# Kernel optimization log

Measured on AMD Instinct MI355X. Metric: run time of the kernel, lower is better.

The kernel has to match this reference:

```python
import jax, jax.numpy as jnp
import numpy as np

N0, N1 = 25000, 25000
N = N0 + N1
E = 600000
D = 128          # in = lattern = hidden = out channels
R = 4            # relations per conv (num_relations // 2)
NB = 4           # num_bases per conv
EPS = 1e-5


def setup_inputs() -> dict:
    key = jax.random.key(0)
    ks = jax.random.split(key, 24)
    inp = {}
    inp['x0'] = jax.random.normal(ks[0], (N0, 128), dtype=jnp.float32)
    inp['x1'] = jax.random.normal(ks[1], (N1, 256), dtype=jnp.float32)
    inp['edge_index'] = jax.random.randint(ks[2], (2, E), 0, N, dtype=jnp.int64)
    inp['edge_type'] = jax.random.randint(ks[3], (E,), 0, 2 * R, dtype=jnp.int64)
    # per-type input projections (torch Linear: y = x @ W.T + b)
    inp['lin0_w'] = jax.random.normal(ks[4], (D, 128), dtype=jnp.float32) * (1.0 / np.sqrt(128))
    inp['lin0_b'] = jnp.zeros((D,), dtype=jnp.float32)
    inp['lin1_w'] = jax.random.normal(ks[5], (D, 256), dtype=jnp.float32) * (1.0 / np.sqrt(256))
    inp['lin1_b'] = jnp.zeros((D,), dtype=jnp.float32)
    # 3 RGCN convs with basis decomposition: weight[r] = sum_b comp[r,b] * bases[b]
    for i, k0 in zip((1, 2, 3), (6, 10, 14)):
        inp[f'comp{i}'] = jax.random.normal(ks[k0], (R, NB), dtype=jnp.float32) * (1.0 / np.sqrt(NB))
        inp[f'bases{i}'] = jax.random.normal(ks[k0 + 1], (NB, D, D), dtype=jnp.float32) * (1.0 / np.sqrt(D))
        inp[f'root{i}'] = jax.random.normal(ks[k0 + 2], (D, D), dtype=jnp.float32) * (1.0 / np.sqrt(D))
        inp[f'b{i}'] = jnp.zeros((D,), dtype=jnp.float32)
    inp['gamma'] = jnp.ones((D,), dtype=jnp.float32)
    inp['beta'] = jnp.zeros((D,), dtype=jnp.float32)
    return inp


def _rgcn_conv(x, src, dst, rel, comp, bases, root, bias):
    # weight: [R, D_in, D_out] via basis decomposition
    W = jnp.einsum('rb,bio->rio', comp, bases)
    out = x @ root + bias  # root/self transform
    xs = x[src]            # [E, D_in] gather (shared across relations)
    for r in range(R):     # small fixed relation count
        mask = (rel == r)
        msg = (xs @ W[r]) * mask[:, None].astype(x.dtype)
        s = jax.ops.segment_sum(msg, dst, num_segments=x.shape[0])
        cnt = jax.ops.segment_sum(mask.astype(x.dtype), dst, num_segments=x.shape[0])
        out = out + s / jnp.maximum(cnt, 1.0)[:, None]  # per-relation scatter-mean
    return out


def reference(x0, x1, edge_index, edge_type,
              lin0_w, lin0_b, lin1_w, lin1_b,
              comp1, bases1, root1, b1,
              comp2, bases2, root2, b2,
              comp3, bases3, root3, b3,
              gamma, beta):
    # trans_dimensions: project each node-type feature matrix, concat on node dim
    x = jnp.concatenate([x0 @ lin0_w.T + lin0_b, x1 @ lin1_w.T + lin1_b], axis=0)
    src, dst = edge_index[0], edge_index[1]
    rel = edge_type // 2
    x = jax.nn.relu(_rgcn_conv(x, src, dst, rel, comp1, bases1, root1, b1))
    # dropout p=0.1: identity in eval mode
    x = jax.nn.relu(_rgcn_conv(x, src, dst, rel, comp2, bases2, root2, b2))
    # dropout p=0.2: identity in eval mode
    x = _rgcn_conv(x, src, dst, rel, comp3, bases3, root3, b3)
    mu = jnp.mean(x, axis=-1, keepdims=True)
    var = jnp.mean(jnp.square(x - mu), axis=-1, keepdims=True)
    return (x - mu) * jax.lax.rsqrt(var + EPS) * gamma + beta
```

## Files before the change

kernel.cpp:

```cpp
#include <hip/hip_runtime.h>


constexpr int cN0 = 25000;
constexpr int cN1 = 25000;
constexpr int cN  = 50000;
constexpr int cE  = 600000;
constexpr int cD  = 128;
constexpr int cR  = 4;
constexpr int cNB = 4;
constexpr int cRN = cR * cN;
constexpr int cSCANBLK = (cRN + 255) / 256;
constexpr int cK  = 640;
constexpr int cWT = cD * cK;

typedef __attribute__((ext_vector_type(8))) short short8v;
typedef __attribute__((ext_vector_type(4))) float float4v;

__device__ inline float bf_hi(float f, short& h)
{
    unsigned u = __float_as_uint(f);
    unsigned r = (u + 0x7fff + ((u >> 16) & 1)) >> 16;
    h = (short)r;
    return __uint_as_float(r << 16);
}

__global__ __launch_bounds__(256)
void build_wt_kernel(const float* __restrict__ c1, const float* __restrict__ ba1, const float* __restrict__ r1,
                     const float* __restrict__ c2, const float* __restrict__ ba2, const float* __restrict__ r2,
                     const float* __restrict__ c3, const float* __restrict__ ba3, const float* __restrict__ r3,
                     short* __restrict__ wt_hi, short* __restrict__ wt_lo)
{
    int idx = blockIdx.x * 256 + threadIdx.x;
    if (idx >= 3 * cWT) return;
    int layer = idx / cWT;
    int rem   = idx - layer * cWT;
    int k     = rem >> 7;
    int col   = rem & 127;
    const float* comp = (layer == 0) ? c1 : (layer == 1) ? c2 : c3;
    const float* bas  = (layer == 0) ? ba1 : (layer == 1) ? ba2 : ba3;
    const float* root = (layer == 0) ? r1 : (layer == 1) ? r2 : r3;
    float v;
    if (k < 128) {
        v = root[k * 128 + col];
    } else {
        int r = (k - 128) >> 7, kk = (k - 128) & 127;
        v = 0.f;
#pragma unroll
        for (int b = 0; b < cNB; ++b)
            v += comp[r * cNB + b] * bas[b * 16384 + kk * 128 + col];
    }
    short h, l;
    float hf = bf_hi(v, h);
    bf_hi(v - hf, l);
    size_t o = (size_t)layer * cWT + (size_t)col * cK + k;
    wt_hi[o] = h;
    wt_lo[o] = l;
}

__global__ __launch_bounds__(256)
void count_kernel(const int* __restrict__ ei, const int* __restrict__ et,
                  int* __restrict__ cnt)
{
    int t = blockIdx.x * 256 + threadIdx.x;
    if (t >= cE) return;
    int dst = ei[cE + t];
    int rel = et[t] >> 1;
    atomicAdd(&cnt[rel * cN + dst], 1);
}

__global__ __launch_bounds__(256)
void scan1_kernel(const int* __restrict__ cnt, int* __restrict__ offs,
                  int* __restrict__ bsum)
{
    __shared__ int s[256];
    int t = threadIdx.x;
    int i = blockIdx.x * 256 + t;
    int v = (i < cRN) ? cnt[i] : 0;
    s[t] = v;
    __syncthreads();
#pragma unroll
    for (int off = 1; off < 256; off <<= 1) {
        int u = (t >= off) ? s[t - off] : 0;
        __syncthreads();
        s[t] += u;
        __syncthreads();
    }
    if (i < cRN) offs[i] = s[t] - v;
    if (t == 255) bsum[blockIdx.x] = s[255];
}

__global__ __launch_bounds__(1024)
void scan2_kernel(int* __restrict__ bsum)
{
    __shared__ int s[1024];
    int t = threadIdx.x;
    int v = (t < cSCANBLK) ? bsum[t] : 0;
    s[t] = v;
    __syncthreads();
#pragma unroll
    for (int off = 1; off < 1024; off <<= 1) {
        int u = (t >= off) ? s[t - off] : 0;
        __syncthreads();
        s[t] += u;
        __syncthreads();
    }
    if (t < cSCANBLK) bsum[t] = s[t] - v;
}

__global__ __launch_bounds__(256)
void scan3_kernel(int* __restrict__ offs, const int* __restrict__ bsum)
{
    int i = blockIdx.x * 256 + threadIdx.x;
    if (i < cRN) offs[i] += bsum[blockIdx.x];
    if (i == 0) offs[cRN] = cE;
}

__global__ __launch_bounds__(256)
void fill_kernel(const int* __restrict__ ei, const int* __restrict__ et,
                 const int* __restrict__ offs, int* __restrict__ fillpos,
                 int* __restrict__ esorted)
{
    int t = blockIdx.x * 256 + threadIdx.x;
    if (t >= cE) return;
    int src = ei[t];
    int dst = ei[cE + t];
    int rel = et[t] >> 1;
    int g = rel * cN + dst;
    int p = atomicAdd(&fillpos[g], 1);
    esorted[offs[g] + p] = src;
}

__global__ __launch_bounds__(256)
void seg_scatter_kernel(const float* __restrict__ x, const int* __restrict__ esorted,
                        const int* __restrict__ offs, float* __restrict__ agg)
{
    int g = blockIdx.x * 4 + (threadIdx.x >> 6);
    if (g >= cRN) return;
    int lane = threadIdx.x & 63;
    int beg = offs[g], end = offs[g + 1];
    float2 acc = {0.f, 0.f};
    for (int j = beg; j < end; ++j) {
        int src = esorted[j];
        const float2 v = *(const float2*)(x + (size_t)src * cD + lane * 2);
        acc.x += v.x;
        acc.y += v.y;
    }
    float invk = 1.0f / fmaxf((float)(end - beg), 1.0f);
    acc.x *= invk;
    acc.y *= invk;
    *(float2*)(agg + (size_t)g * cD + lane * 2) = acc;
}

template<int EPI>
__global__ __launch_bounds__(512)
void mfma_conv_kernel(const float* __restrict__ x,
                      const float* __restrict__ agg,
                      const short* __restrict__ wt_hi,
                      const short* __restrict__ wt_lo,
                      const float* __restrict__ bias,
                      float* __restrict__ out)
{
    __shared__ short As_hi[128][32];
    __shared__ short As_lo[128][32];
    __shared__ short Bs_hi[128][32];
    __shared__ short Bs_lo[128][32];

    const int tid  = threadIdx.x;
    const int row0 = blockIdx.x * 128;

    const int srow = tid >> 2;
    const int sk8  = (tid & 3) * 8;
    const int gi   = row0 + srow;

    const int lane = tid & 63;
    const int wid  = tid >> 6;
    const int wm   = wid >> 2;
    const int wn   = wid & 3;
    const int fr   = lane & 15;
    const int fk   = (lane >> 4) * 8;

    float4v acc[4][2];
#pragma unroll
    for (int m = 0; m < 4; ++m)
#pragma unroll
        for (int n = 0; n < 2; ++n)
#pragma unroll
            for (int r = 0; r < 4; ++r) acc[m][n][r] = 0.f;

#pragma unroll 1
    for (int st = 0; st < 20; ++st) {
        const int s  = st >> 2;
        const int k0 = (st & 3) * 32;

        short8v vh, vl;
        if (gi < cN) {
            const float* src = (s == 0)
                ? (x + (size_t)gi * cD + k0 + sk8)
                : (agg + ((size_t)(s - 1) * cN + gi) * cD + k0 + sk8);
            float4 a = *(const float4*)(src);
            float4 b = *(const float4*)(src + 4);
            float vv[8] = {a.x, a.y, a.z, a.w, b.x, b.y, b.z, b.w};
#pragma unroll
            for (int j = 0; j < 8; ++j) {
                short h, l;
                float hf = bf_hi(vv[j], h);
                bf_hi(vv[j] - hf, l);
                vh[j] = h;
                vl[j] = l;
            }
        } else {
#pragma unroll
            for (int j = 0; j < 8; ++j) { vh[j] = 0; vl[j] = 0; }
        }
        *(short8v*)&As_hi[srow][sk8] = vh;
        *(short8v*)&As_lo[srow][sk8] = vl;

        const int kglob = st * 32 + sk8;
        *(short8v*)&Bs_hi[srow][sk8] = *(const short8v*)(wt_hi + (size_t)srow * cK + kglob);
        *(short8v*)&Bs_lo[srow][sk8] = *(const short8v*)(wt_lo + (size_t)srow * cK + kglob);

        __syncthreads();

        short8v ah[4], al[4], bh[2], bl[2];
#pragma unroll
        for (int mf = 0; mf < 4; ++mf) {
            ah[mf] = *(const short8v*)&As_hi[wm * 64 + mf * 16 + fr][fk];
            al[mf] = *(const short8v*)&As_lo[wm * 64 + mf * 16 + fr][fk];
        }
#pragma unroll
        for (int nf = 0; nf < 2; ++nf) {
            bh[nf] = *(const short8v*)&Bs_hi[wn * 32 + nf * 16 + fr][fk];
            bl[nf] = *(const short8v*)&Bs_lo[wn * 32 + nf * 16 + fr][fk];
        }

#pragma unroll
        for (int mf = 0; mf < 4; ++mf)
#pragma unroll
            for (int nf = 0; nf < 2; ++nf) {
                acc[mf][nf] = __builtin_amdgcn_mfma_f32_16x16x32_bf16(al[mf], bh[nf], acc[mf][nf], 0, 0, 0);
                acc[mf][nf] = __builtin_amdgcn_mfma_f32_16x16x32_bf16(ah[mf], bl[nf], acc[mf][nf], 0, 0, 0);
                acc[mf][nf] = __builtin_amdgcn_mfma_f32_16x16x32_bf16(ah[mf], bh[nf], acc[mf][nf], 0, 0, 0);
            }

        __syncthreads();
    }

#pragma unroll
    for (int mf = 0; mf < 4; ++mf)
#pragma unroll
        for (int nf = 0; nf < 2; ++nf) {
            int col = wn * 32 + nf * 16 + fr;
            float bi = bias[col];
#pragma unroll
            for (int r = 0; r < 4; ++r) {
                int gr = row0 + wm * 64 + mf * 16 + (lane >> 4) * 4 + r;
                if (gr < cN) {
                    float v = acc[mf][nf][r] + bi;
                    if (EPI == 1) v = fmaxf(v, 0.f);
                    out[(size_t)gr * cD + col] = v;
                }
            }
        }
}

__global__ __launch_bounds__(256)
void ln_kernel(float* __restrict__ io, const float* __restrict__ gamma,
               const float* __restrict__ beta)
{
    int row = blockIdx.x * 4 + (threadIdx.x >> 6);
    if (row >= cN) return;
    int lane = threadIdx.x & 63;
    float2 v = *(const float2*)(io + (size_t)row * cD + lane * 2);
    float sm = v.x + v.y;
#pragma unroll
    for (int off = 1; off < 64; off <<= 1) sm += __shfl_xor(sm, off, 64);
    float mu = sm * (1.0f / 128.0f);
    float dx = v.x - mu, dy = v.y - mu;
    float sq = dx * dx + dy * dy;
#pragma unroll
    for (int off = 1; off < 64; off <<= 1) sq += __shfl_xor(sq, off, 64);
    float rs = rsqrtf(sq * (1.0f / 128.0f) + 1e-5f);
    float2 g = *(const float2*)(gamma + lane * 2);
    float2 b = *(const float2*)(beta + lane * 2);
    float2 o;
    o.x = dx * rs * g.x + b.x;
    o.y = dy * rs * g.y + b.y;
    *(float2*)(io + (size_t)row * cD + lane * 2) = o;
}

template<int NSEG>
__global__ __launch_bounds__(256)
void proj_gemm_kernel(const float* __restrict__ A0,
                      const float* __restrict__ B0,
                      const float* __restrict__ bias,
                      float* __restrict__ out,
                      int M)
{
    __shared__ float As[32][128];
    __shared__ float Bs[32][128];

    const int tid = threadIdx.x;
    const int tx = tid & 15;
    const int ty = tid >> 4;
    const int row0 = blockIdx.x * 128;

    float acc[8][8];
#pragma unroll
    for (int m = 0; m < 8; ++m)
#pragma unroll
        for (int n = 0; n < 8; ++n) acc[m][n] = 0.f;

    const int iloc = tid & 127;
    const int kh   = tid >> 7;
    const int gi   = row0 + iloc;

#pragma unroll 1
    for (int ch = 0; ch < NSEG * 4; ++ch) {
        const int s  = ch >> 2;
        const int k0 = (ch & 3) * 32;

        if (gi < M) {
            const float* src = A0 + (size_t)gi * (NSEG * 128) + s * 128 + k0 + kh * 16;
#pragma unroll
            for (int j = 0; j < 4; ++j) {
                float4 t4 = *(const float4*)(src + j * 4);
                As[kh * 16 + j * 4 + 0][iloc] = t4.x;
                As[kh * 16 + j * 4 + 1][iloc] = t4.y;
                As[kh * 16 + j * 4 + 2][iloc] = t4.z;
                As[kh * 16 + j * 4 + 3][iloc] = t4.w;
            }
        } else {
#pragma unroll
            for (int j = 0; j < 16; ++j) As[kh * 16 + j][iloc] = 0.f;
        }

        {
            const int o = iloc;
            const float* p = B0 + (size_t)o * (NSEG * 128) + s * 128 + k0 + kh * 16;
#pragma unroll
            for (int j = 0; j < 4; ++j) {
                float4 t4 = *(const float4*)(p + j * 4);
                Bs[kh * 16 + j * 4 + 0][o] = t4.x;
                Bs[kh * 16 + j * 4 + 1][o] = t4.y;
                Bs[kh * 16 + j * 4 + 2][o] = t4.z;
                Bs[kh * 16 + j * 4 + 3][o] = t4.w;
            }
        }
        __syncthreads();

#pragma unroll
        for (int kk = 0; kk < 32; ++kk) {
            float a[8], b[8];
            *(float4*)&a[0] = *(const float4*)&As[kk][ty * 8];
            *(float4*)&a[4] = *(const float4*)&As[kk][ty * 8 + 4];
            *(float4*)&b[0] = *(const float4*)&Bs[kk][tx * 8];
            *(float4*)&b[4] = *(const float4*)&Bs[kk][tx * 8 + 4];
#pragma unroll
            for (int m = 0; m < 8; ++m)
#pragma unroll
                for (int n = 0; n < 8; ++n)
                    acc[m][n] = fmaf(a[m], b[n], acc[m][n]);
        }
        __syncthreads();
    }

    float bi[8];
    *(float4*)&bi[0] = *(const float4*)(bias + tx * 8);
    *(float4*)&bi[4] = *(const float4*)(bias + tx * 8 + 4);

#pragma unroll
    for (int m = 0; m < 8; ++m) {
        int gr = row0 + ty * 8 + m;
        if (gr < M) {
            float v[8];
#pragma unroll
            for (int n = 0; n < 8; ++n) v[n] = acc[m][n] + bi[n];
            float4* o0 = (float4*)(out + (size_t)gr * 128 + tx * 8);
            o0[0] = *(float4*)&v[0];
            o0[1] = *(float4*)&v[4];
        }
    }
}

extern "C" void kernel_launch(void* const* d_in, const int* in_sizes, int n_in,
                              void* d_out, int out_size, void* d_ws, size_t ws_size,
                              hipStream_t stream)
{
    (void)in_sizes; (void)n_in; (void)out_size; (void)ws_size;

    const float* x0     = (const float*)d_in[0];
    const float* x1     = (const float*)d_in[1];
    const int*   ei     = (const int*)d_in[2];
    const int*   et     = (const int*)d_in[3];
    const float* lin0_w = (const float*)d_in[4];
    const float* lin0_b = (const float*)d_in[5];
    const float* lin1_w = (const float*)d_in[6];
    const float* lin1_b = (const float*)d_in[7];
    const float* comp1  = (const float*)d_in[8];
    const float* bases1 = (const float*)d_in[9];
    const float* root1  = (const float*)d_in[10];
    const float* b1     = (const float*)d_in[11];
    const float* comp2  = (const float*)d_in[12];
    const float* bases2 = (const float*)d_in[13];
    const float* root2  = (const float*)d_in[14];
    const float* b2     = (const float*)d_in[15];
    const float* comp3  = (const float*)d_in[16];
    const float* bases3 = (const float*)d_in[17];
    const float* root3  = (const float*)d_in[18];
    const float* b3     = (const float*)d_in[19];
    const float* gamma  = (const float*)d_in[20];
    const float* beta   = (const float*)d_in[21];

    float* out = (float*)d_out;

    char* ws = (char*)d_ws;
    size_t off = 0;
    auto alloc = [&](size_t bytes) {
        void* p = ws + off;
        off = (off + bytes + 255) & ~(size_t)255;
        return p;
    };
    float* xbuf    = (float*)alloc((size_t)cN * cD * 4);
    float* agg     = (float*)alloc((size_t)cR * cN * cD * 4);
    short* wt_hi   = (short*)alloc((size_t)3 * cWT * 2);
    short* wt_lo   = (short*)alloc((size_t)3 * cWT * 2);
    int*   offs    = (int*)alloc((size_t)(cRN + 1) * 4);
    int*   cnt     = (int*)alloc((size_t)cRN * 4);
    int*   bsum    = (int*)alloc((size_t)cSCANBLK * 4);
    int*   esorted = (int*)alloc((size_t)cE * 4);

    build_wt_kernel<<<(3 * cWT + 255) / 256, 256, 0, stream>>>(
        comp1, bases1, root1, comp2, bases2, root2, comp3, bases3, root3,
        wt_hi, wt_lo);
    hipMemsetAsync(cnt, 0, (size_t)cRN * 4, stream);
    count_kernel<<<(cE + 255) / 256, 256, 0, stream>>>(ei, et, cnt);
    scan1_kernel<<<cSCANBLK, 256, 0, stream>>>(cnt, offs, bsum);
    scan2_kernel<<<1, 1024, 0, stream>>>(bsum);
    scan3_kernel<<<cSCANBLK, 256, 0, stream>>>(offs, bsum);
    hipMemsetAsync(cnt, 0, (size_t)cRN * 4, stream);
    fill_kernel<<<(cE + 255) / 256, 256, 0, stream>>>(ei, et, offs, cnt, esorted);

    proj_gemm_kernel<1><<<(cN0 + 127) / 128, 256, 0, stream>>>(
        x0, lin0_w, lin0_b, xbuf, cN0);
    proj_gemm_kernel<2><<<(cN1 + 127) / 128, 256, 0, stream>>>(
        x1, lin1_w, lin1_b, xbuf + (size_t)cN0 * cD, cN1);

    const int convGrid = (cN + 127) / 128;

    seg_scatter_kernel<<<(cRN + 3) / 4, 256, 0, stream>>>(xbuf, esorted, offs, agg);
    mfma_conv_kernel<1><<<convGrid, 512, 0, stream>>>(
        xbuf, agg, wt_hi + (size_t)0 * cWT, wt_lo + (size_t)0 * cWT, b1, out);

    seg_scatter_kernel<<<(cRN + 3) / 4, 256, 0, stream>>>(out, esorted, offs, agg);
    mfma_conv_kernel<1><<<convGrid, 512, 0, stream>>>(
        out, agg, wt_hi + (size_t)1 * cWT, wt_lo + (size_t)1 * cWT, b2, xbuf);

    seg_scatter_kernel<<<(cRN + 3) / 4, 256, 0, stream>>>(xbuf, esorted, offs, agg);
    mfma_conv_kernel<0><<<convGrid, 512, 0, stream>>>(
        xbuf, agg, wt_hi + (size_t)2 * cWT, wt_lo + (size_t)2 * cWT, b3, out);
    ln_kernel<<<(cN + 3) / 4, 256, 0, stream>>>(out, gamma, beta);
}
```

Baseline: 647.2 us.

## Batch edge index loads with shuffles and swizzle LDS tiles in MFMA conv

The segment scatter kernel now loads up to 64 source indices at once with one coalesced wave load, broadcasts them with shuffles, and issues four row gathers per iteration. This raises memory-level parallelism and removes the serial index-load dependency. Separately, the MFMA GEMM kernel XOR-swizzles the LDS column offsets for the A and B tiles to cut bank conflicts on the short8 reads. The added shuffles and predicated adds cost a few instructions per edge.

```diff
diff --git a/kernel.cpp b/kernel.cpp
--- a/kernel.cpp
+++ b/kernel.cpp
@@ -138,14 +138,34 @@
     if (g >= cRN) return;
     int lane = threadIdx.x & 63;
     int beg = offs[g], end = offs[g + 1];
+    int n = end - beg;
     float2 acc = {0.f, 0.f};
-    for (int j = beg; j < end; ++j) {
-        int src = esorted[j];
-        const float2 v = *(const float2*)(x + (size_t)src * cD + lane * 2);
-        acc.x += v.x;
-        acc.y += v.y;
-    }
-    float invk = 1.0f / fmaxf((float)(end - beg), 1.0f);
+    const float* xl = x + lane * 2;
+
+    for (int base = 0; base < n; base += 64) {
+        int m = n - base;
+        if (m > 64) m = 64;
+        int idx = (lane < m) ? esorted[beg + base + lane] : 0;
+        for (int jb = 0; jb < m; jb += 4) {
+            int j1 = (jb + 1 < m) ? jb + 1 : jb;
+            int j2 = (jb + 2 < m) ? jb + 2 : jb;
+            int j3 = (jb + 3 < m) ? jb + 3 : jb;
+            int s0 = __shfl(idx, jb, 64);
+            int s1 = __shfl(idx, j1, 64);
+            int s2 = __shfl(idx, j2, 64);
+            int s3 = __shfl(idx, j3, 64);
+            float2 v0 = *(const float2*)(xl + (size_t)s0 * cD);
+            float2 v1 = *(const float2*)(xl + (size_t)s1 * cD);
+            float2 v2 = *(const float2*)(xl + (size_t)s2 * cD);
+            float2 v3 = *(const float2*)(xl + (size_t)s3 * cD);
+            acc.x += v0.x;
+            acc.y += v0.y;
+            if (jb + 1 < m) { acc.x += v1.x; acc.y += v1.y; }
+            if (jb + 2 < m) { acc.x += v2.x; acc.y += v2.y; }
+            if (jb + 3 < m) { acc.x += v3.x; acc.y += v3.y; }
+        }
+    }
+    float invk = 1.0f / fmaxf((float)n, 1.0f);
     acc.x *= invk;
     acc.y *= invk;
     *(float2*)(agg + (size_t)g * cD + lane * 2) = acc;
@@ -170,6 +190,7 @@
 
     const int srow = tid >> 2;
     const int sk8  = (tid & 3) * 8;
+    const int scol = sk8 ^ (((srow >> 1) & 3) << 3);
     const int gi   = row0 + srow;
 
     const int lane = tid & 63;
@@ -212,25 +233,29 @@
 #pragma unroll
             for (int j = 0; j < 8; ++j) { vh[j] = 0; vl[j] = 0; }
         }
-        *(short8v*)&As_hi[srow][sk8] = vh;
-        *(short8v*)&As_lo[srow][sk8] = vl;
+        *(short8v*)&As_hi[srow][scol] = vh;
+        *(short8v*)&As_lo[srow][scol] = vl;
 
         const int kglob = st * 32 + sk8;
-        *(short8v*)&Bs_hi[srow][sk8] = *(const short8v*)(wt_hi + (size_t)srow * cK + kglob);
-        *(short8v*)&Bs_lo[srow][sk8] = *(const short8v*)(wt_lo + (size_t)srow * cK + kglob);
+        *(short8v*)&Bs_hi[srow][scol] = *(const short8v*)(wt_hi + (size_t)srow * cK + kglob);
+        *(short8v*)&Bs_lo[srow][scol] = *(const short8v*)(wt_lo + (size_t)srow * cK + kglob);
 
         __syncthreads();
 
         short8v ah[4], al[4], bh[2], bl[2];
 #pragma unroll
         for (int mf = 0; mf < 4; ++mf) {
-            ah[mf] = *(const short8v*)&As_hi[wm * 64 + mf * 16 + fr][fk];
-            al[mf] = *(const short8v*)&As_lo[wm * 64 + mf * 16 + fr][fk];
+            int arow = wm * 64 + mf * 16 + fr;
+            int acol = fk ^ (((arow >> 1) & 3) << 3);
+            ah[mf] = *(const short8v*)&As_hi[arow][acol];
+            al[mf] = *(const short8v*)&As_lo[arow][acol];
         }
 #pragma unroll
         for (int nf = 0; nf < 2; ++nf) {
-            bh[nf] = *(const short8v*)&Bs_hi[wn * 32 + nf * 16 + fr][fk];
-            bl[nf] = *(const short8v*)&Bs_lo[wn * 32 + nf * 16 + fr][fk];
+            int brow = wn * 32 + nf * 16 + fr;
+            int bcol = fk ^ (((brow >> 1) & 3) << 3);
+            bh[nf] = *(const short8v*)&Bs_hi[brow][bcol];
+            bl[nf] = *(const short8v*)&Bs_lo[brow][bcol];
         }
 
 #pragma unroll
```

Result: faster. 579.4 us (-10.5%).
